# Performance work log

Measured on AMD Instinct MI355X. Metric: run time of the kernel, lower is better.

## Reference

```python
import jax, jax.numpy as jnp
import numpy as np

N_NODES = 50000
IN_DIM = 128
HID = 2 * IN_DIM  # 256, per module: hidden_dim = input_dims * 2
FC1 = 1024
FC2 = 512
N_ACT = 64
N_EDGES = 800000
N_AGENTS = 16384


def _layernorm(h, g, b, eps=1e-5):
    mu = jnp.mean(h, axis=-1, keepdims=True)
    var = jnp.var(h, axis=-1, keepdims=True)
    return (h - mu) * jax.lax.rsqrt(var + eps) * g + b


def setup_inputs() -> dict:
    key = jax.random.key(0)
    ks = jax.random.split(key, 16)
    def u(k, shape, fan_in):
        s = 1.0 / np.sqrt(fan_in)
        return jax.random.uniform(k, shape, jnp.float32, -s, s)
    inp = {}
    inp["x"] = jax.random.normal(ks[0], (N_NODES, IN_DIM), jnp.float32)
    inp["action"] = jax.random.normal(ks[1], (N_AGENTS, N_ACT), jnp.float32)
    inp["edge_index"] = jax.random.randint(ks[2], (2, N_EDGES), 0, N_NODES, jnp.int32)
    inp["agent_idx"] = jax.random.randint(ks[3], (N_AGENTS,), 0, N_NODES, jnp.int32)
    # GCNConv params (linear no bias + separate bias)
    inp["W_gcn"] = u(ks[4], (IN_DIM, HID), IN_DIM)
    inp["b_gcn"] = jnp.zeros((HID,), jnp.float32)
    # fc1, fc2 (custom uniform init per module)
    inp["W1"] = u(ks[5], (HID, FC1), FC1)
    inp["b1"] = u(ks[6], (FC1,), FC1)
    inp["g1"] = jnp.ones((FC1,), jnp.float32)
    inp["beta1"] = jnp.zeros((FC1,), jnp.float32)
    inp["W2"] = u(ks[7], (FC1, FC2), FC2)
    inp["b2"] = u(ks[8], (FC2,), FC2)
    inp["g2"] = jnp.ones((FC2,), jnp.float32)
    inp["beta2"] = jnp.zeros((FC2,), jnp.float32)
    inp["Wa"] = u(ks[9], (N_ACT, FC2), FC2)
    inp["ba"] = u(ks[10], (FC2,), FC2)
    inp["Wq"] = jax.random.uniform(ks[11], (FC2, 1), jnp.float32, -0.003, 0.003)
    inp["bq"] = jax.random.uniform(ks[12], (1,), jnp.float32, -0.003, 0.003)
    return inp


def reference(x, action, W_gcn, b_gcn, W1, b1, g1, beta1, W2, b2, g2, beta2, Wa, ba, Wq, bq, edge_index, agent_idx):
    N = x.shape[0]
    # GCNConv: add self-loops, symmetric D^-1/2 (A+I) D^-1/2 normalization
    loops = jnp.arange(N, dtype=edge_index.dtype)
    src = jnp.concatenate([edge_index[0], loops])
    dst = jnp.concatenate([edge_index[1], loops])
    h = x @ W_gcn  # [N, HID] transform before aggregation
    deg = jax.ops.segment_sum(jnp.ones_like(dst, dtype=h.dtype), dst, num_segments=N)
    dinv = jax.lax.rsqrt(jnp.maximum(deg, 1.0))  # deg >= 1 due to self-loops
    norm = dinv[src] * dinv[dst]  # [E+N]
    agg = jax.ops.segment_sum(h[src] * norm[:, None], dst, num_segments=N) + b_gcn
    # masked gather of agent nodes, then critic MLP
    z = jax.nn.relu(agg[agent_idx])  # [A, HID]
    s = jax.nn.relu(_layernorm(z @ W1 + b1, g1, beta1))
    s = _layernorm(s @ W2 + b2, g2, beta2)
    a = action @ Wa + ba
    sa = jax.nn.relu(s + a)
    return sa @ Wq + bq  # [A, 1]
```

## Files before the change

kernel.cpp:

```cpp
#include <hip/hip_runtime.h>
#include <hip/hip_bf16.h>

typedef _Float16 f16;
typedef _Float16 __attribute__((ext_vector_type(8))) half8;
typedef _Float16 __attribute__((ext_vector_type(4))) half4;
typedef float __attribute__((ext_vector_type(4))) floatx4;

#define IN_DIM 128
#define HID    256
#define FC1    1024
#define FC2    512
#define NACT   64
#define BUCKET 128

__global__ void prep0_kernel(int* degcnt, int* needed, int* n_needed, int* cursor, int N, int A) {
    int b = blockIdx.x, tid = threadIdx.x;
    if (b < 196) {
        int i = b * 256 + tid;
        if (i < N) { degcnt[i] = 0; needed[i] = 0; }
        if (b == 0 && tid == 0) *n_needed = 0;
        return;
    }
    b -= 196;
    cursor[b * 256 + tid] = 0;
}

__device__ __forceinline__ void transpose_tile(const float* __restrict__ in, f16* __restrict__ out,
                                               int K, int N, int bx, int by, int tid) {
    __shared__ f16 tile[32][33];
    int k0 = bx * 32, n0 = by * 32;
    int tx = tid & 31, ty = tid >> 5;
    #pragma unroll
    for (int i = 0; i < 4; ++i)
        tile[ty + i * 8][tx] = (f16)in[(size_t)(k0 + ty + i * 8) * N + n0 + tx];
    __syncthreads();
    #pragma unroll
    for (int i = 0; i < 4; ++i)
        out[(size_t)(n0 + ty + i * 8) * K + k0 + tx] = tile[tx][ty + i * 8];
}

__device__ __forceinline__ void cvt8(const float* __restrict__ in, f16* __restrict__ out, long gi) {
    float4 a = *(const float4*)&in[gi * 8];
    float4 b = *(const float4*)&in[gi * 8 + 4];
    half8 pk;
    pk[0] = (f16)a.x; pk[1] = (f16)a.y; pk[2] = (f16)a.z; pk[3] = (f16)a.w;
    pk[4] = (f16)b.x; pk[5] = (f16)b.y; pk[6] = (f16)b.z; pk[7] = (f16)b.w;
    *(half8*)&out[gi * 8] = pk;
}

__global__ __launch_bounds__(256)
void prep1_kernel(const float* __restrict__ Wgcn, const float* __restrict__ W1,
                  const float* __restrict__ W2, const float* __restrict__ Wa,
                  const float* __restrict__ action, const int* __restrict__ agent_idx,
                  f16* WgcnT, f16* W1T, f16* W2T, f16* WaT, f16* act16,
                  int* needed, int* needed_list, int* n_needed, int A) {
    int b = blockIdx.x, tid = threadIdx.x;
    if (b < 32)  { transpose_tile(Wgcn, WgcnT, IN_DIM, HID, b & 3, b >> 2, tid); return; }
    b -= 32;
    if (b < 256) { transpose_tile(W1, W1T, HID, FC1, b & 7, b >> 3, tid); return; }
    b -= 256;
    if (b < 512) { transpose_tile(W2, W2T, FC1, FC2, b & 31, b >> 5, tid); return; }
    b -= 512;
    if (b < 32)  { transpose_tile(Wa, WaT, NACT, FC2, b & 1, b >> 1, tid); return; }
    b -= 32;
    if (b < 512) { cvt8(action, act16, (long)b * 256 + tid); return; }
    b -= 512;
    int i = b * 256 + tid;
    if (i < A) {
        int idx = agent_idx[i];
        if (atomicCAS(&needed[idx], 0, -1) == 0) {
            int p = atomicAdd(n_needed, 1);
            needed_list[p] = idx;
            needed[idx] = p + 1;
        }
    }
}

__global__ void degfill_kernel(const int* __restrict__ esrc, const int* __restrict__ edst,
                               const int* __restrict__ needed, int* __restrict__ degcnt,
                               int* __restrict__ cursor, int* __restrict__ srcbuf, int E) {
    int e = blockIdx.x * 256 + threadIdx.x;
    if (e < E) {
        int d = edst[e];
        atomicAdd(&degcnt[d], 1);
        int s = needed[d];
        if (s != 0) {
            int slot = s - 1;
            int pos = atomicAdd(&cursor[slot], 1);
            if (pos < BUCKET) srcbuf[(size_t)slot * BUCKET + pos] = esrc[e];
        }
    }
}

__global__ __launch_bounds__(256)
void gather_x_kernel(const int* __restrict__ needed_list, const int* __restrict__ n_needed,
                     const int* __restrict__ degcnt, const int* __restrict__ srcbuf,
                     const float* __restrict__ x, f16* __restrict__ xagg) {
    int w = (blockIdx.x * 256 + threadIdx.x) >> 6;
    int lane = threadIdx.x & 63;
    if (w >= *n_needed) return;
    int d = needed_list[w];
    float dd = rsqrtf((float)degcnt[d] + 1.0f);
    size_t beg = (size_t)w * BUCKET;
    int cnt = degcnt[d];
    if (cnt > BUCKET) cnt = BUCKET;
    float2 xs = *(const float2*)&x[(size_t)d * IN_DIM + lane * 2];
    float ax = xs.x * dd * dd, ay = xs.y * dd * dd;
    int j = 0;
    for (; j + 3 < cnt; j += 4) {
        int s0 = srcbuf[beg + j], s1 = srcbuf[beg + j + 1];
        int s2 = srcbuf[beg + j + 2], s3 = srcbuf[beg + j + 3];
        float n0 = rsqrtf((float)degcnt[s0] + 1.0f) * dd;
        float n1 = rsqrtf((float)degcnt[s1] + 1.0f) * dd;
        float n2 = rsqrtf((float)degcnt[s2] + 1.0f) * dd;
        float n3 = rsqrtf((float)degcnt[s3] + 1.0f) * dd;
        float2 v0 = *(const float2*)&x[(size_t)s0 * IN_DIM + lane * 2];
        float2 v1 = *(const float2*)&x[(size_t)s1 * IN_DIM + lane * 2];
        float2 v2 = *(const float2*)&x[(size_t)s2 * IN_DIM + lane * 2];
        float2 v3 = *(const float2*)&x[(size_t)s3 * IN_DIM + lane * 2];
        ax = fmaf(v0.x, n0, ax); ay = fmaf(v0.y, n0, ay);
        ax = fmaf(v1.x, n1, ax); ay = fmaf(v1.y, n1, ay);
        ax = fmaf(v2.x, n2, ax); ay = fmaf(v2.y, n2, ay);
        ax = fmaf(v3.x, n3, ax); ay = fmaf(v3.y, n3, ay);
    }
    for (; j < cnt; ++j) {
        int s0 = srcbuf[beg + j];
        float n0 = rsqrtf((float)degcnt[s0] + 1.0f) * dd;
        float2 v0 = *(const float2*)&x[(size_t)s0 * IN_DIM + lane * 2];
        ax = fmaf(v0.x, n0, ax);
        ay = fmaf(v0.y, n0, ay);
    }
    union { f16 h[2]; unsigned u; } pk;
    pk.h[0] = (f16)ax; pk.h[1] = (f16)ay;
    *(unsigned*)&xagg[(size_t)w * IN_DIM + lane * 2] = pk.u;
}

__device__ __forceinline__ void swz_decode(int bid, int log2ny, int& bx, int& by) {
    int xcd = bid & 7;
    int pos = bid >> 3;
    bx = (pos >> log2ny) * 8 + xcd;
    by = pos & ((1 << log2ny) - 1);
}

template<bool RELU, bool LIMIT>
__device__ __forceinline__ void gemm_tile64(f16* __restrict__ smA, f16* __restrict__ smB,
                                            const f16* __restrict__ A, const f16* __restrict__ BT,
                                            f16* __restrict__ C, const float* __restrict__ bias,
                                            const int* __restrict__ limit,
                                            int bx, int by, int N, int K) {
    if (LIMIT && bx * 64 >= *limit) return;
    const int tid = threadIdx.x;
    const int lane = tid & 63;
    const int wave = tid >> 6;
    const int wr = wave >> 1, wc = wave & 1;
    const long bm = (long)bx * 64, bn = (long)by * 64;

    size_t aoff[2], boff[2];
    #pragma unroll
    for (int t = 0; t < 2; ++t) {
        int ci = t * 256 + tid;
        int r = ci >> 3, s = ci & 7, ks = s ^ (r & 7);
        aoff[t] = (size_t)(bm + r) * K + ks * 8;
        boff[t] = (size_t)(bn + r) * K + ks * 8;
    }
    int aidx[2][2], bidx[2][2];
    const int kc = lane >> 4;
    #pragma unroll
    for (int kk = 0; kk < 2; ++kk) {
        #pragma unroll
        for (int i = 0; i < 2; ++i) {
            int ar = wr * 32 + i * 16 + (lane & 15);
            aidx[kk][i] = ar * 64 + ((kk * 4 + kc) ^ (ar & 7)) * 8;
            int br = wc * 32 + i * 16 + (lane & 15);
            bidx[kk][i] = br * 64 + ((kk * 4 + kc) ^ (br & 7)) * 8;
        }
    }

    const int NT = K >> 6;
    auto stage = [&](int buf, int k0) {
        #pragma unroll
        for (int t = 0; t < 2; ++t) {
            __builtin_amdgcn_global_load_lds(
                (const __attribute__((address_space(1))) void*)(A + aoff[t] + k0),
                (__attribute__((address_space(3))) void*)(&smA[buf * 4096 + (t * 256 + tid) * 8]), 16, 0, 0);
            __builtin_amdgcn_global_load_lds(
                (const __attribute__((address_space(1))) void*)(BT + boff[t] + k0),
                (__attribute__((address_space(3))) void*)(&smB[buf * 4096 + (t * 256 + tid) * 8]), 16, 0, 0);
        }
    };

    floatx4 acc[2][2] = {};
    stage(0, 0);
    asm volatile("s_waitcnt vmcnt(0)" ::: "memory");
    __builtin_amdgcn_s_barrier();
    int cur = 0;
    for (int t = 0; t < NT; ++t) {
        if (t + 1 < NT) stage(cur ^ 1, (t + 1) << 6);
        #pragma unroll
        for (int kk = 0; kk < 2; ++kk) {
            half8 af[2], bf[2];
            #pragma unroll
            for (int i = 0; i < 2; ++i) {
                af[i] = *(const half8*)&smA[cur * 4096 + aidx[kk][i]];
                bf[i] = *(const half8*)&smB[cur * 4096 + bidx[kk][i]];
            }
            #pragma unroll
            for (int mi = 0; mi < 2; ++mi)
                #pragma unroll
                for (int ni = 0; ni < 2; ++ni)
                    acc[mi][ni] = __builtin_amdgcn_mfma_f32_16x16x32_f16(af[mi], bf[ni], acc[mi][ni], 0, 0, 0);
        }
        asm volatile("s_waitcnt vmcnt(0)" ::: "memory");
        __builtin_amdgcn_s_barrier();
        cur ^= 1;
    }
    f16* scr = smA + wave * 512;
    #pragma unroll
    for (int mi = 0; mi < 2; ++mi) {
        __syncthreads();
        #pragma unroll
        for (int ni = 0; ni < 2; ++ni) {
            int c = ni * 16 + (lane & 15);
            float bz = bias[bn + wc * 32 + c];
            #pragma unroll
            for (int q = 0; q < 4; ++q) {
                int r = (lane >> 4) * 4 + q;
                float v = acc[mi][ni][q] + bz;
                if (RELU) v = fmaxf(v, 0.f);
                scr[r * 32 + c] = (f16)v;
            }
        }
        __syncthreads();
        int r = lane >> 2, ch = lane & 3;
        half8 v = *(const half8*)&scr[r * 32 + ch * 8];
        *(half8*)&C[(size_t)(bm + wr * 32 + mi * 16 + r) * N + (bn + wc * 32 + ch * 8)] = v;
    }
}

template<bool RELU, bool LIMIT>
__global__ __launch_bounds__(256)
void gemm64_kernel(const f16* __restrict__ A, const f16* __restrict__ BT,
                   f16* __restrict__ C, const float* __restrict__ bias,
                   const int* __restrict__ limit, int N, int K, int log2ny) {
    __shared__ __align__(16) f16 smA[2 * 4096];
    __shared__ __align__(16) f16 smB[2 * 4096];
    int bx, by;
    swz_decode(blockIdx.x, log2ny, bx, by);
    gemm_tile64<RELU, LIMIT>(smA, smB, A, BT, C, bias, limit, bx, by, N, K);
}

template<bool LIMIT>
__device__ __forceinline__ void gemm_tile128(f16* __restrict__ smA, f16* __restrict__ smB,
                                             const f16* __restrict__ A, const f16* __restrict__ BT,
                                             f16* __restrict__ C, const float* __restrict__ bias,
                                             const int* __restrict__ limit,
                                             int bx, int by, int N, int K) {
    if (LIMIT && bx * 128 >= *limit) return;
    const int tid = threadIdx.x;
    const int lane = tid & 63;
    const int wave = tid >> 6;
    const int wr = wave >> 1, wc = wave & 1;
    const long bm = (long)bx * 128, bn = (long)by * 128;

    size_t aoff[4], boff[4];
    #pragma unroll
    for (int t = 0; t < 4; ++t) {
        int ci = t * 256 + tid;
        int r = ci >> 3, s = ci & 7, ks = s ^ (r & 7);
        aoff[t] = (size_t)(bm + r) * K + ks * 8;
        boff[t] = (size_t)(bn + r) * K + ks * 8;
    }
    int aidx[2][4], bidx[2][4];
    const int kc = lane >> 4;
    #pragma unroll
    for (int kk = 0; kk < 2; ++kk) {
        #pragma unroll
        for (int i = 0; i < 4; ++i) {
            int ar = wr * 64 + i * 16 + (lane & 15);
            aidx[kk][i] = ar * 64 + ((kk * 4 + kc) ^ (ar & 7)) * 8;
            int br = wc * 64 + i * 16 + (lane & 15);
            bidx[kk][i] = br * 64 + ((kk * 4 + kc) ^ (br & 7)) * 8;
        }
    }

    const int NT = K >> 6;
    auto stage = [&](int buf, int k0) {
        #pragma unroll
        for (int t = 0; t < 4; ++t) {
            __builtin_amdgcn_global_load_lds(
                (const __attribute__((address_space(1))) void*)(A + aoff[t] + k0),
                (__attribute__((address_space(3))) void*)(&smA[buf * 8192 + (t * 256 + tid) * 8]), 16, 0, 0);
            __builtin_amdgcn_global_load_lds(
                (const __attribute__((address_space(1))) void*)(BT + boff[t] + k0),
                (__attribute__((address_space(3))) void*)(&smB[buf * 8192 + (t * 256 + tid) * 8]), 16, 0, 0);
        }
    };

    floatx4 acc[4][4] = {};
    stage(0, 0);
    asm volatile("s_waitcnt vmcnt(0)" ::: "memory");
    __builtin_amdgcn_s_barrier();
    int cur = 0;
    for (int t = 0; t < NT; ++t) {
        if (t + 1 < NT) stage(cur ^ 1, (t + 1) << 6);
        #pragma unroll
        for (int kk = 0; kk < 2; ++kk) {
            half8 af[4], bf[4];
            #pragma unroll
            for (int i = 0; i < 4; ++i) {
                af[i] = *(const half8*)&smA[cur * 8192 + aidx[kk][i]];
                bf[i] = *(const half8*)&smB[cur * 8192 + bidx[kk][i]];
            }
            #pragma unroll
            for (int mi = 0; mi < 4; ++mi)
                #pragma unroll
                for (int ni = 0; ni < 4; ++ni)
                    acc[mi][ni] = __builtin_amdgcn_mfma_f32_16x16x32_f16(af[mi], bf[ni], acc[mi][ni], 0, 0, 0);
        }
        asm volatile("s_waitcnt vmcnt(0)" ::: "memory");
        __builtin_amdgcn_s_barrier();
        cur ^= 1;
    }
    f16* scr = smA + wave * 1024;
    #pragma unroll
    for (int mi = 0; mi < 4; ++mi) {
        __syncthreads();
        #pragma unroll
        for (int ni = 0; ni < 4; ++ni) {
            int c = ni * 16 + (lane & 15);
            float bz = bias[bn + wc * 64 + c];
            #pragma unroll
            for (int q = 0; q < 4; ++q) {
                int r = (lane >> 4) * 4 + q;
                scr[r * 64 + c] = (f16)(acc[mi][ni][q] + bz);
            }
        }
        __syncthreads();
        #pragma unroll
        for (int it = 0; it < 2; ++it) {
            int flat = it * 64 + lane;
            int r = flat >> 3, ch = flat & 7;
            half8 v = *(const half8*)&scr[r * 64 + ch * 8];
            *(half8*)&C[(size_t)(bm + wr * 64 + mi * 16 + r) * N + (bn + wc * 64 + ch * 8)] = v;
        }
    }
}

template<bool LIMIT>
__global__ __launch_bounds__(256)
void gemm128_kernel(const f16* __restrict__ A, const f16* __restrict__ BT,
                    f16* __restrict__ C, const float* __restrict__ bias,
                    const int* __restrict__ limit, int N, int K, int log2ny) {
    __shared__ __align__(16) f16 smA[2 * 8192];
    __shared__ __align__(16) f16 smB[2 * 8192];
    int bx, by;
    swz_decode(blockIdx.x, log2ny, bx, by);
    gemm_tile128<LIMIT>(smA, smB, A, BT, C, bias, limit, bx, by, N, K);
}

__global__ __launch_bounds__(256)
void gemm_dual_kernel(const f16* __restrict__ A0, const f16* __restrict__ BT0, f16* __restrict__ C0,
                      const float* __restrict__ bias0, const int* __restrict__ limit, int K0,
                      const f16* __restrict__ A1, const f16* __restrict__ BT1, f16* __restrict__ C1,
                      const float* __restrict__ bias1, int K1, int half, int N) {
    __shared__ __align__(16) f16 smA[2 * 8192];
    __shared__ __align__(16) f16 smB[2 * 8192];
    int bid = blockIdx.x;
    int bx, by;
    if (bid < half) {
        swz_decode(bid, 2, bx, by);
        gemm_tile128<true>(smA, smB, A0, BT0, C0, bias0, limit, bx, by, N, K0);
    } else {
        swz_decode(bid - half, 2, bx, by);
        gemm_tile128<false>(smA, smB, A1, BT1, C1, bias1, nullptr, bx, by, N, K1);
    }
}

__global__ __launch_bounds__(256)
void ln_relu_f16_kernel(f16* __restrict__ s, const float* __restrict__ g,
                        const float* __restrict__ b, const int* __restrict__ nn) {
    int row = blockIdx.x;
    if (row >= *nn) return;
    f16* p = s + (size_t)row * FC1;
    int tid = threadIdx.x;
    half4 v = *(const half4*)&p[tid * 4];
    float f0 = (float)v[0], f1 = (float)v[1], f2 = (float)v[2], f3 = (float)v[3];
    float sum = f0 + f1 + f2 + f3;
    float sq = f0 * f0 + f1 * f1 + f2 * f2 + f3 * f3;
    #pragma unroll
    for (int off = 32; off > 0; off >>= 1) {
        sum += __shfl_down(sum, off);
        sq  += __shfl_down(sq, off);
    }
    __shared__ float ssum[4], ssq[4];
    int wid = tid >> 6;
    if ((tid & 63) == 0) { ssum[wid] = sum; ssq[wid] = sq; }
    __syncthreads();
    float tot = ssum[0] + ssum[1] + ssum[2] + ssum[3];
    float tq  = ssq[0] + ssq[1] + ssq[2] + ssq[3];
    float mu = tot * (1.0f / FC1);
    float var = tq * (1.0f / FC1) - mu * mu;
    float rs = rsqrtf(var + 1e-5f);
    float4 gg = *(const float4*)&g[tid * 4];
    float4 bb = *(const float4*)&b[tid * 4];
    half4 o;
    o[0] = (f16)fmaxf((f0 - mu) * rs * gg.x + bb.x, 0.f);
    o[1] = (f16)fmaxf((f1 - mu) * rs * gg.y + bb.y, 0.f);
    o[2] = (f16)fmaxf((f2 - mu) * rs * gg.z + bb.z, 0.f);
    o[3] = (f16)fmaxf((f3 - mu) * rs * gg.w + bb.w, 0.f);
    *(half4*)&p[tid * 4] = o;
}

__global__ __launch_bounds__(256)
void final_f16_kernel(const f16* __restrict__ s2, const f16* __restrict__ ab,
                      const int* __restrict__ agent_idx, const int* __restrict__ needed,
                      const float* __restrict__ g2, const float* __restrict__ b2,
                      const float* __restrict__ Wq, const float* __restrict__ bq,
                      float* __restrict__ out) {
    int row = blockIdx.x;
    int slot = needed[agent_idx[row]] - 1;
    const f16* p = s2 + (size_t)slot * FC2;
    int tid = threadIdx.x;
    float v0 = (float)p[tid * 2], v1 = (float)p[tid * 2 + 1];
    float sum = v0 + v1;
    float sq = v0 * v0 + v1 * v1;
    #pragma unroll
    for (int off = 32; off > 0; off >>= 1) {
        sum += __shfl_down(sum, off);
        sq  += __shfl_down(sq, off);
    }
    __shared__ float ssum[4], ssq[4], spart[4];
    int wid = tid >> 6;
    if ((tid & 63) == 0) { ssum[wid] = sum; ssq[wid] = sq; }
    __syncthreads();
    float tot = ssum[0] + ssum[1] + ssum[2] + ssum[3];
    float tq  = ssq[0] + ssq[1] + ssq[2] + ssq[3];
    float mu = tot * (1.0f / FC2);
    float var = tq * (1.0f / FC2) - mu * mu;
    float rs = rsqrtf(var + 1e-5f);
    float a0 = (float)ab[(size_t)row * FC2 + tid * 2];
    float a1 = (float)ab[(size_t)row * FC2 + tid * 2 + 1];
    float g0 = g2[tid * 2], g1 = g2[tid * 2 + 1];
    float bb0 = b2[tid * 2], bb1 = b2[tid * 2 + 1];
    float sa0 = fmaxf((v0 - mu) * rs * g0 + bb0 + a0, 0.f);
    float sa1 = fmaxf((v1 - mu) * rs * g1 + bb1 + a1, 0.f);
    float part = sa0 * Wq[tid * 2] + sa1 * Wq[tid * 2 + 1];
    #pragma unroll
    for (int off = 32; off > 0; off >>= 1) part += __shfl_down(part, off);
    if ((tid & 63) == 0) spart[wid] = part;
    __syncthreads();
    if (tid == 0) out[row] = spart[0] + spart[1] + spart[2] + spart[3] + bq[0];
}

extern "C" void kernel_launch(void* const* d_in, const int* in_sizes, int n_in,
                              void* d_out, int out_size, void* d_ws, size_t ws_size,
                              hipStream_t stream) {
    const float* x        = (const float*)d_in[0];
    const float* action   = (const float*)d_in[1];
    const int*   edge     = (const int*)d_in[2];
    const int*   agent_idx= (const int*)d_in[3];
    const float* W_gcn    = (const float*)d_in[4];
    const float* b_gcn    = (const float*)d_in[5];
    const float* W1       = (const float*)d_in[6];
    const float* b1       = (const float*)d_in[7];
    const float* g1       = (const float*)d_in[8];
    const float* beta1    = (const float*)d_in[9];
    const float* W2       = (const float*)d_in[10];
    const float* b2       = (const float*)d_in[11];
    const float* g2       = (const float*)d_in[12];
    const float* beta2    = (const float*)d_in[13];
    const float* Wa       = (const float*)d_in[14];
    const float* ba       = (const float*)d_in[15];
    const float* Wq       = (const float*)d_in[16];
    const float* bq       = (const float*)d_in[17];
    float* out = (float*)d_out;

    const int N = in_sizes[0] / IN_DIM;
    const int E = in_sizes[2] / 2;
    const int A = in_sizes[3];
    const int* esrc = edge;
    const int* edst = edge + E;

    char* ws = (char*)d_ws;
    size_t off = 0;
    auto carve = [&](size_t bytes) -> char* {
        char* p = ws + off;
        off += (bytes + 255) & ~(size_t)255;
        return p;
    };
    int*   degcnt     = (int*)  carve((size_t)N * 4);
    int*   needed     = (int*)  carve((size_t)N * 4);
    int*   cursor     = (int*)  carve((size_t)A * 4);
    int*   needed_list= (int*)  carve((size_t)A * 4);
    int*   n_needed   = (int*)  carve(256);
    int*   srcbuf     = (int*)  carve((size_t)A * BUCKET * 4);
    f16*   WgcnT      = (f16*)  carve((size_t)HID * IN_DIM * 2);
    f16*   W1T        = (f16*)  carve((size_t)FC1 * HID * 2);
    f16*   W2T        = (f16*)  carve((size_t)FC2 * FC1 * 2);
    f16*   WaT        = (f16*)  carve((size_t)FC2 * NACT * 2);
    f16*   act16      = (f16*)  carve((size_t)A * NACT * 2);
    f16*   xagg       = (f16*)  carve((size_t)A * IN_DIM * 2);
    f16*   z          = (f16*)  carve((size_t)A * HID * 2);
    f16*   s1         = (f16*)  carve((size_t)A * FC1 * 2);
    f16*   s2         = (f16*)  carve((size_t)A * FC2 * 2);
    f16*   abuf       = (f16*)  carve((size_t)A * FC2 * 2);
    (void)ws_size;

    const int eblk = (E + 255) / 256;

    prep0_kernel<<<196 + 64, 256, 0, stream>>>(degcnt, needed, n_needed, cursor, N, A);
    prep1_kernel<<<32 + 256 + 512 + 32 + 512 + 64, 256, 0, stream>>>(
        W_gcn, W1, W2, Wa, action, agent_idx,
        WgcnT, W1T, W2T, WaT, act16, needed, needed_list, n_needed, A);
    degfill_kernel<<<eblk, 256, 0, stream>>>(esrc, edst, needed, degcnt, cursor, srcbuf, E);
    gather_x_kernel<<<(A + 3) / 4, 256, 0, stream>>>(needed_list, n_needed, degcnt,
                                                     srcbuf, x, xagg);
    gemm64_kernel<true, true><<<(A / 64) * (HID / 64), 256, 0, stream>>>(
        xagg, WgcnT, z, b_gcn, n_needed, HID, IN_DIM, 2);
    gemm128_kernel<true><<<(A / 128) * (FC1 / 128), 256, 0, stream>>>(
        z, W1T, s1, b1, n_needed, FC1, HID, 3);
    ln_relu_f16_kernel<<<A, 256, 0, stream>>>(s1, g1, beta1, n_needed);
    gemm_dual_kernel<<<2 * (A / 128) * (FC2 / 128), 256, 0, stream>>>(
        s1, W2T, s2, b2, n_needed, FC1,
        act16, WaT, abuf, ba, NACT, (A / 128) * (FC2 / 128), FC2);
    final_f16_kernel<<<A, 256, 0, stream>>>(s2, abuf, agent_idx, needed, g2, beta2, Wq, bq, out);
}
```

Before: 160.5 us.

## Overlap action GEMM with edge degree fill and cut duplicate atomics

Moves the action@Wa GEMM out of the dual GEMM launch and runs it in the same grid as the edge-scan degree/bucket fill, so the compute-bound GEMM tiles overlap with the atomic-bound edge pass. The edge pass now issues only one atomic per edge: needed nodes get their degree from the bucket cursor instead of a separate degcnt increment. The gather kernel resolves each source degree through the needed map, which adds an extra dependent load per neighbour. The W2 GEMM becomes a plain 128-tile launch.

```diff
diff --git a/kernel.cpp b/kernel.cpp
--- a/kernel.cpp
+++ b/kernel.cpp
@@ -76,65 +76,6 @@
     }
 }
 
-__global__ void degfill_kernel(const int* __restrict__ esrc, const int* __restrict__ edst,
-                               const int* __restrict__ needed, int* __restrict__ degcnt,
-                               int* __restrict__ cursor, int* __restrict__ srcbuf, int E) {
-    int e = blockIdx.x * 256 + threadIdx.x;
-    if (e < E) {
-        int d = edst[e];
-        atomicAdd(&degcnt[d], 1);
-        int s = needed[d];
-        if (s != 0) {
-            int slot = s - 1;
-            int pos = atomicAdd(&cursor[slot], 1);
-            if (pos < BUCKET) srcbuf[(size_t)slot * BUCKET + pos] = esrc[e];
-        }
-    }
-}
-
-__global__ __launch_bounds__(256)
-void gather_x_kernel(const int* __restrict__ needed_list, const int* __restrict__ n_needed,
-                     const int* __restrict__ degcnt, const int* __restrict__ srcbuf,
-                     const float* __restrict__ x, f16* __restrict__ xagg) {
-    int w = (blockIdx.x * 256 + threadIdx.x) >> 6;
-    int lane = threadIdx.x & 63;
-    if (w >= *n_needed) return;
-    int d = needed_list[w];
-    float dd = rsqrtf((float)degcnt[d] + 1.0f);
-    size_t beg = (size_t)w * BUCKET;
-    int cnt = degcnt[d];
-    if (cnt > BUCKET) cnt = BUCKET;
-    float2 xs = *(const float2*)&x[(size_t)d * IN_DIM + lane * 2];
-    float ax = xs.x * dd * dd, ay = xs.y * dd * dd;
-    int j = 0;
-    for (; j + 3 < cnt; j += 4) {
-        int s0 = srcbuf[beg + j], s1 = srcbuf[beg + j + 1];
-        int s2 = srcbuf[beg + j + 2], s3 = srcbuf[beg + j + 3];
-        float n0 = rsqrtf((float)degcnt[s0] + 1.0f) * dd;
-        float n1 = rsqrtf((float)degcnt[s1] + 1.0f) * dd;
-        float n2 = rsqrtf((float)degcnt[s2] + 1.0f) * dd;
-        float n3 = rsqrtf((float)degcnt[s3] + 1.0f) * dd;
-        float2 v0 = *(const float2*)&x[(size_t)s0 * IN_DIM + lane * 2];
-        float2 v1 = *(const float2*)&x[(size_t)s1 * IN_DIM + lane * 2];
-        float2 v2 = *(const float2*)&x[(size_t)s2 * IN_DIM + lane * 2];
-        float2 v3 = *(const float2*)&x[(size_t)s3 * IN_DIM + lane * 2];
-        ax = fmaf(v0.x, n0, ax); ay = fmaf(v0.y, n0, ay);
-        ax = fmaf(v1.x, n1, ax); ay = fmaf(v1.y, n1, ay);
-        ax = fmaf(v2.x, n2, ax); ay = fmaf(v2.y, n2, ay);
-        ax = fmaf(v3.x, n3, ax); ay = fmaf(v3.y, n3, ay);
-    }
-    for (; j < cnt; ++j) {
-        int s0 = srcbuf[beg + j];
-        float n0 = rsqrtf((float)degcnt[s0] + 1.0f) * dd;
-        float2 v0 = *(const float2*)&x[(size_t)s0 * IN_DIM + lane * 2];
-        ax = fmaf(v0.x, n0, ax);
-        ay = fmaf(v0.y, n0, ay);
-    }
-    union { f16 h[2]; unsigned u; } pk;
-    pk.h[0] = (f16)ax; pk.h[1] = (f16)ay;
-    *(unsigned*)&xagg[(size_t)w * IN_DIM + lane * 2] = pk.u;
-}
-
 __device__ __forceinline__ void swz_decode(int bid, int log2ny, int& bx, int& by) {
     int xcd = bid & 7;
     int pos = bid >> 3;
@@ -249,6 +190,85 @@
     gemm_tile64<RELU, LIMIT>(smA, smB, A, BT, C, bias, limit, bx, by, N, K);
 }
 
+__global__ __launch_bounds__(256)
+void degfill_abuf_kernel(const int* __restrict__ esrc, const int* __restrict__ edst,
+                         const int* __restrict__ needed, int* __restrict__ degcnt,
+                         int* __restrict__ cursor, int* __restrict__ srcbuf,
+                         const f16* __restrict__ act16, const f16* __restrict__ WaT,
+                         f16* __restrict__ abuf, const float* __restrict__ ba,
+                         int E, int gblk) {
+    __shared__ __align__(16) f16 smA[2 * 4096];
+    __shared__ __align__(16) f16 smB[2 * 4096];
+    int b = blockIdx.x;
+    if (b < gblk) {
+        int bx, by;
+        swz_decode(b, 3, bx, by);
+        gemm_tile64<false, false>(smA, smB, act16, WaT, abuf, ba, nullptr, bx, by, FC2, NACT);
+        return;
+    }
+    int e = (b - gblk) * 256 + threadIdx.x;
+    if (e < E) {
+        int d = edst[e];
+        int s = needed[d];
+        if (s == 0) {
+            atomicAdd(&degcnt[d], 1);
+        } else {
+            int slot = s - 1;
+            int pos = atomicAdd(&cursor[slot], 1);
+            if (pos < BUCKET) srcbuf[(size_t)slot * BUCKET + pos] = esrc[e];
+        }
+    }
+}
+
+__global__ __launch_bounds__(256)
+void gather_x_kernel(const int* __restrict__ needed_list, const int* __restrict__ n_needed,
+                     const int* __restrict__ needed, const int* __restrict__ degcnt,
+                     const int* __restrict__ cursor, const int* __restrict__ srcbuf,
+                     const float* __restrict__ x, f16* __restrict__ xagg) {
+    int w = (blockIdx.x * 256 + threadIdx.x) >> 6;
+    int lane = threadIdx.x & 63;
+    if (w >= *n_needed) return;
+    int d = needed_list[w];
+    int degd = cursor[w];
+    float dd = rsqrtf((float)degd + 1.0f);
+    size_t beg = (size_t)w * BUCKET;
+    int cnt = degd < BUCKET ? degd : BUCKET;
+    float2 xs = *(const float2*)&x[(size_t)d * IN_DIM + lane * 2];
+    float ax = xs.x * dd * dd, ay = xs.y * dd * dd;
+    auto src_deg = [&](int s) -> float {
+        int ns = needed[s];
+        int dg = (ns != 0) ? cursor[ns - 1] : degcnt[s];
+        return (float)dg;
+    };
+    int j = 0;
+    for (; j + 3 < cnt; j += 4) {
+        int s0 = srcbuf[beg + j], s1 = srcbuf[beg + j + 1];
+        int s2 = srcbuf[beg + j + 2], s3 = srcbuf[beg + j + 3];
+        float n0 = rsqrtf(src_deg(s0) + 1.0f) * dd;
+        float n1 = rsqrtf(src_deg(s1) + 1.0f) * dd;
+        float n2 = rsqrtf(src_deg(s2) + 1.0f) * dd;
+        float n3 = rsqrtf(src_deg(s3) + 1.0f) * dd;
+        float2 v0 = *(const float2*)&x[(size_t)s0 * IN_DIM + lane * 2];
+        float2 v1 = *(const float2*)&x[(size_t)s1 * IN_DIM + lane * 2];
+        float2 v2 = *(const float2*)&x[(size_t)s2 * IN_DIM + lane * 2];
+        float2 v3 = *(const float2*)&x[(size_t)s3 * IN_DIM + lane * 2];
+        ax = fmaf(v0.x, n0, ax); ay = fmaf(v0.y, n0, ay);
+        ax = fmaf(v1.x, n1, ax); ay = fmaf(v1.y, n1, ay);
+        ax = fmaf(v2.x, n2, ax); ay = fmaf(v2.y, n2, ay);
+        ax = fmaf(v3.x, n3, ax); ay = fmaf(v3.y, n3, ay);
+    }
+    for (; j < cnt; ++j) {
+        int s0 = srcbuf[beg + j];
+        float n0 = rsqrtf(src_deg(s0) + 1.0f) * dd;
+        float2 v0 = *(const float2*)&x[(size_t)s0 * IN_DIM + lane * 2];
+        ax = fmaf(v0.x, n0, ax);
+        ay = fmaf(v0.y, n0, ay);
+    }
+    union { f16 h[2]; unsigned u; } pk;
+    pk.h[0] = (f16)ax; pk.h[1] = (f16)ay;
+    *(unsigned*)&xagg[(size_t)w * IN_DIM + lane * 2] = pk.u;
+}
+
 template<bool LIMIT>
 __device__ __forceinline__ void gemm_tile128(f16* __restrict__ smA, f16* __restrict__ smB,
                                              const f16* __restrict__ A, const f16* __restrict__ BT,
@@ -356,24 +376,6 @@
     int bx, by;
     swz_decode(blockIdx.x, log2ny, bx, by);
     gemm_tile128<LIMIT>(smA, smB, A, BT, C, bias, limit, bx, by, N, K);
-}
-
-__global__ __launch_bounds__(256)
-void gemm_dual_kernel(const f16* __restrict__ A0, const f16* __restrict__ BT0, f16* __restrict__ C0,
-                      const float* __restrict__ bias0, const int* __restrict__ limit, int K0,
-                      const f16* __restrict__ A1, const f16* __restrict__ BT1, f16* __restrict__ C1,
-                      const float* __restrict__ bias1, int K1, int half, int N) {
-    __shared__ __align__(16) f16 smA[2 * 8192];
-    __shared__ __align__(16) f16 smB[2 * 8192];
-    int bid = blockIdx.x;
-    int bx, by;
-    if (bid < half) {
-        swz_decode(bid, 2, bx, by);
-        gemm_tile128<true>(smA, smB, A0, BT0, C0, bias0, limit, bx, by, N, K0);
-    } else {
-        swz_decode(bid - half, 2, bx, by);
-        gemm_tile128<false>(smA, smB, A1, BT1, C1, bias1, nullptr, bx, by, N, K1);
-    }
 }
 
 __global__ __launch_bounds__(256)
@@ -507,21 +509,23 @@
     (void)ws_size;
 
     const int eblk = (E + 255) / 256;
+    const int gblk = (A / 64) * (FC2 / 64);
 
     prep0_kernel<<<196 + 64, 256, 0, stream>>>(degcnt, needed, n_needed, cursor, N, A);
     prep1_kernel<<<32 + 256 + 512 + 32 + 512 + 64, 256, 0, stream>>>(
         W_gcn, W1, W2, Wa, action, agent_idx,
         WgcnT, W1T, W2T, WaT, act16, needed, needed_list, n_needed, A);
-    degfill_kernel<<<eblk, 256, 0, stream>>>(esrc, edst, needed, degcnt, cursor, srcbuf, E);
-    gather_x_kernel<<<(A + 3) / 4, 256, 0, stream>>>(needed_list, n_needed, degcnt,
-                                                     srcbuf, x, xagg);
+    degfill_abuf_kernel<<<gblk + eblk, 256, 0, stream>>>(
+        esrc, edst, needed, degcnt, cursor, srcbuf,
+        act16, WaT, abuf, ba, E, gblk);
+    gather_x_kernel<<<(A + 3) / 4, 256, 0, stream>>>(needed_list, n_needed, needed,
+                                                     degcnt, cursor, srcbuf, x, xagg);
     gemm64_kernel<true, true><<<(A / 64) * (HID / 64), 256, 0, stream>>>(
         xagg, WgcnT, z, b_gcn, n_needed, HID, IN_DIM, 2);
     gemm128_kernel<true><<<(A / 128) * (FC1 / 128), 256, 0, stream>>>(
         z, W1T, s1, b1, n_needed, FC1, HID, 3);
     ln_relu_f16_kernel<<<A, 256, 0, stream>>>(s1, g1, beta1, n_needed);
-    gemm_dual_kernel<<<2 * (A / 128) * (FC2 / 128), 256, 0, stream>>>(
-        s1, W2T, s2, b2, n_needed, FC1,
-        act16, WaT, abuf, ba, NACT, (A / 128) * (FC2 / 128), FC2);
+    gemm128_kernel<true><<<(A / 128) * (FC2 / 128), 256, 0, stream>>>(
+        s1, W2T, s2, b2, n_needed, FC2, FC1, 2);
     final_f16_kernel<<<A, 256, 0, stream>>>(s2, abuf, agent_idx, needed, g2, beta2, Wq, bq, out);
 }
```

Result: faster. 154.6 us (-3.7%).
